# Kernel tuning notes

Measured on AMD Instinct MI355X. Metric: run time of the kernel, lower is better.

The kernel has to match this reference:

```python
import jax, jax.numpy as jnp
import numpy as np

# neighbor-sampled node counts per hop level (outermost -> batch)
SIZES = (1363968, 123904, 11264, 1024)
E = (1239040, 112640, 10240)
D_IN, D_H, D_OUT = 128, 256, 64


def _sage(x_src, x_dst, src, dst, Wl, bl, Wr):
    """PyG SAGEConv(aggr='mean') on bipartite (x_src, x_dst) graph."""
    n_dst = x_dst.shape[0]
    agg = jax.ops.segment_sum(x_src[src], dst, num_segments=n_dst)
    cnt = jax.ops.segment_sum(jnp.ones((src.shape[0],), x_src.dtype), dst, num_segments=n_dst)
    mean = agg / jnp.maximum(cnt, 1.0)[:, None]
    return mean @ Wl + bl + x_dst @ Wr  # lin_l(mean) + lin_r(x_dst), lin_r has no bias


def setup_inputs() -> dict:
    key = jax.random.key(0)
    ks = jax.random.split(key, 16)
    inp = {}
    inp["x"] = jax.random.normal(ks[0], (SIZES[0], D_IN), dtype=jnp.float32)
    dims = [(D_IN, D_H), (D_H, D_H), (D_H, D_OUT)]
    for i, (di, do) in enumerate(dims):
        s = 1.0 / np.sqrt(di)
        inp[f"Wl{i}"] = jax.random.uniform(ks[1 + 3 * i], (di, do), jnp.float32, -s, s)
        inp[f"bl{i}"] = jax.random.uniform(ks[2 + 3 * i], (do,), jnp.float32, -s, s)
        inp[f"Wr{i}"] = jax.random.uniform(ks[3 + 3 * i], (di, do), jnp.float32, -s, s)
    for i in range(3):
        inp[f"edge_src{i}"] = jax.random.randint(ks[10 + i * 2], (E[i],), 0, SIZES[i], dtype=jnp.int32)
        inp[f"edge_dst{i}"] = jax.random.randint(ks[11 + i * 2 - 1], (E[i],), 0, SIZES[i + 1], dtype=jnp.int32)
    return inp


def reference(x, Wl0, bl0, Wr0, Wl1, bl1, Wr1, Wl2, bl2, Wr2,
              edge_src0, edge_dst0, edge_src1, edge_dst1, edge_src2, edge_dst2):
    # layer 0 (i=0 != num_layers-1=1 -> relu; dropout is identity in eval)
    h = _sage(x, x[:SIZES[1]], edge_src0, edge_dst0, Wl0, bl0, Wr0)
    h = jax.nn.relu(h)
    # layer 1 (i=1 == num_layers-1 -> no relu)
    h = _sage(h, h[:SIZES[2]], edge_src1, edge_dst1, Wl1, bl1, Wr1)
    # layer 2 (i=2 != 1 -> relu, faithful to the original quirk)
    h = _sage(h, h[:SIZES[3]], edge_src2, edge_dst2, Wl2, bl2, Wr2)
    h = jax.nn.relu(h)
    return h
```

## Files before the change

### kernel.cpp

```cpp
#include <hip/hip_runtime.h>

#define SZ0 1363968
#define SZ1 123904
#define SZ2 11264
#define SZ3 1024
#define NE0 1239040
#define NE1 112640
#define NE2 10240
#define DIN 128
#define DH  256
#define DOUT 64

__global__ __launch_bounds__(256) void hist_all(
    const int* __restrict__ ed0, const int* __restrict__ ed1,
    const int* __restrict__ ed2, int* __restrict__ bk0,
    int* __restrict__ bk1, int* __restrict__ bk2)
{
    int e = blockIdx.x * 256 + threadIdx.x;
    if (e < NE0) {
        atomicAdd(&bk0[ed0[e]], 1);
    } else if (e < NE0 + NE1) {
        atomicAdd(&bk1[ed1[e - NE0]], 1);
    } else {
        atomicAdd(&bk2[ed2[e - NE0 - NE1]], 1);
    }
}

__global__ __launch_bounds__(1024) void scan_all(
    int* __restrict__ a0, int n0, int* __restrict__ a1, int n1,
    int* __restrict__ a2, int n2)
{
    __shared__ int sums[1024];
    int* a; int n;
    if (blockIdx.x == 0)      { a = a0; n = n0; }
    else if (blockIdx.x == 1) { a = a1; n = n1; }
    else                      { a = a2; n = n2; }

    const int t = threadIdx.x;
    const int C = (n + 1023) >> 10;
    const int lo = t * C;
    const int hi = min(lo + C, n);
    int s = 0;
    for (int i = lo; i < hi; i++) s += a[i];
    sums[t] = s;
    __syncthreads();
    for (int off = 1; off < 1024; off <<= 1) {
        int v = (t >= off) ? sums[t - off] : 0;
        __syncthreads();
        sums[t] += v;
        __syncthreads();
    }
    int pre = (t == 0) ? 0 : sums[t - 1];
    for (int i = lo; i < hi; i++) { int v = a[i]; a[i] = pre; pre += v; }
}

__global__ __launch_bounds__(256) void bucket_all(
    const int* __restrict__ es0, const int* __restrict__ ed0,
    const int* __restrict__ es1, const int* __restrict__ ed1,
    const int* __restrict__ es2, const int* __restrict__ ed2,
    int* __restrict__ bk0, int* __restrict__ bk1, int* __restrict__ bk2,
    int* __restrict__ p0, int* __restrict__ p1, int* __restrict__ p2)
{
    int e = blockIdx.x * 256 + threadIdx.x;
    if (e < NE0) {
        int pos = atomicAdd(&bk0[ed0[e]], 1);
        p0[pos] = es0[e];
    } else if (e < NE0 + NE1) {
        int i = e - NE0;
        int pos = atomicAdd(&bk1[ed1[i]], 1);
        p1[pos] = es1[i];
    } else {
        int i = e - NE0 - NE1;
        int pos = atomicAdd(&bk2[ed2[i]], 1);
        p2[pos] = es2[i];
    }
}

template <int D>
__global__ __launch_bounds__(256) void gather_mean(
    const float* __restrict__ X, const int* __restrict__ perm,
    const int* __restrict__ ends, float* __restrict__ out)
{
    constexpr int VEC = D / 64;
    const int wave = (blockIdx.x * 256 + threadIdx.x) >> 6;
    const int lane = threadIdx.x & 63;
    const int start = (wave == 0) ? 0 : ends[wave - 1];
    const int end = ends[wave];

    float acc[4][VEC];
#pragma unroll
    for (int u = 0; u < 4; u++)
#pragma unroll
        for (int i = 0; i < VEC; i++) acc[u][i] = 0.0f;

    int e = start;
    for (; e + 4 <= end; e += 4) {
        int s0 = perm[e], s1 = perm[e + 1], s2 = perm[e + 2], s3 = perm[e + 3];
        const float* p0 = X + (size_t)s0 * D + lane * VEC;
        const float* p1 = X + (size_t)s1 * D + lane * VEC;
        const float* p2 = X + (size_t)s2 * D + lane * VEC;
        const float* p3 = X + (size_t)s3 * D + lane * VEC;
        if (VEC == 2) {
            float2 v0 = *reinterpret_cast<const float2*>(p0);
            float2 v1 = *reinterpret_cast<const float2*>(p1);
            float2 v2 = *reinterpret_cast<const float2*>(p2);
            float2 v3 = *reinterpret_cast<const float2*>(p3);
            acc[0][0] += v0.x; acc[0][1] += v0.y;
            acc[1][0] += v1.x; acc[1][1] += v1.y;
            acc[2][0] += v2.x; acc[2][1] += v2.y;
            acc[3][0] += v3.x; acc[3][1] += v3.y;
        } else {
            float4 v0 = *reinterpret_cast<const float4*>(p0);
            float4 v1 = *reinterpret_cast<const float4*>(p1);
            float4 v2 = *reinterpret_cast<const float4*>(p2);
            float4 v3 = *reinterpret_cast<const float4*>(p3);
            acc[0][0] += v0.x; acc[0][1] += v0.y; acc[0][2] += v0.z; acc[0][3] += v0.w;
            acc[1][0] += v1.x; acc[1][1] += v1.y; acc[1][2] += v1.z; acc[1][3] += v1.w;
            acc[2][0] += v2.x; acc[2][1] += v2.y; acc[2][2] += v2.z; acc[2][3] += v2.w;
            acc[3][0] += v3.x; acc[3][1] += v3.y; acc[3][2] += v3.z; acc[3][3] += v3.w;
        }
    }
    for (; e < end; e++) {
        int s0 = perm[e];
        const float* p0 = X + (size_t)s0 * D + lane * VEC;
        if (VEC == 2) {
            float2 v0 = *reinterpret_cast<const float2*>(p0);
            acc[0][0] += v0.x; acc[0][1] += v0.y;
        } else {
            float4 v0 = *reinterpret_cast<const float4*>(p0);
            acc[0][0] += v0.x; acc[0][1] += v0.y; acc[0][2] += v0.z; acc[0][3] += v0.w;
        }
    }

    const float inv = 1.0f / (float)max(end - start, 1);
    float* o = out + (size_t)wave * D + lane * VEC;
    if (VEC == 2) {
        float2 v;
        v.x = (acc[0][0] + acc[1][0] + acc[2][0] + acc[3][0]) * inv;
        v.y = (acc[0][1] + acc[1][1] + acc[2][1] + acc[3][1]) * inv;
        *reinterpret_cast<float2*>(o) = v;
    } else {
        float4 v;
        v.x = (acc[0][0] + acc[1][0] + acc[2][0] + acc[3][0]) * inv;
        v.y = (acc[0][1] + acc[1][1] + acc[2][1] + acc[3][1]) * inv;
        v.z = (acc[0][2] + acc[1][2] + acc[2][2] + acc[3][2]) * inv;
        v.w = (acc[0][3] + acc[1][3] + acc[2][3] + acc[3][3]) * inv;
        *reinterpret_cast<float4*>(o) = v;
    }
}

template <int BM, int BN>
__global__ __launch_bounds__(256) void gemm_sage(
    const float* __restrict__ A1, const float* __restrict__ A2,
    const float* __restrict__ B1, const float* __restrict__ B2,
    const float* __restrict__ bias, float* __restrict__ C,
    int K1, int K2, int do_relu)
{
    constexpr int BK = 32;
    constexpr int ROWS = BM / 16;
    constexpr int G = BN / 64;
    constexpr int AF4 = (BM * 8) / 256;
    constexpr int BF4 = (BN * 8) / 256;

    __shared__ float As[BK][BM + 4];
    __shared__ float Bs[BK][BN + 4];

    const int tid = threadIdx.x;
    const int m0 = blockIdx.x * BM;
    const int ty = tid >> 4;
    const int tx = tid & 15;

    float acc[ROWS][G * 4];
#pragma unroll
    for (int i = 0; i < ROWS; i++)
#pragma unroll
        for (int j = 0; j < G * 4; j++) acc[i][j] = 0.0f;

    const int K = K1 + K2;
    for (int kt = 0; kt < K; kt += BK) {
        const float* Ap; const float* Bp; int lK, kof;
        if (kt < K1) { Ap = A1; Bp = B1; lK = K1; kof = kt; }
        else         { Ap = A2; Bp = B2; lK = K2; kof = kt - K1; }

#pragma unroll
        for (int j = 0; j < AF4; j++) {
            int id = tid * AF4 + j;
            int m = id >> 3;
            int q = id & 7;
            float4 v = *reinterpret_cast<const float4*>(
                Ap + (size_t)(m0 + m) * lK + kof + q * 4);
            As[q * 4 + 0][m] = v.x;
            As[q * 4 + 1][m] = v.y;
            As[q * 4 + 2][m] = v.z;
            As[q * 4 + 3][m] = v.w;
        }
#pragma unroll
        for (int j = 0; j < BF4; j++) {
            int id = tid * BF4 + j;
            int k = id / (BN / 4);
            int c = id % (BN / 4);
            float4 v = *reinterpret_cast<const float4*>(
                Bp + (size_t)(kof + k) * BN + c * 4);
            *reinterpret_cast<float4*>(&Bs[k][c * 4]) = v;
        }
        __syncthreads();

#pragma unroll
        for (int kk = 0; kk < BK; kk++) {
            float a[ROWS];
            if constexpr (ROWS == 4) {
                float4 av = *reinterpret_cast<const float4*>(&As[kk][ty * 4]);
                a[0] = av.x; a[1] = av.y; a[2] = av.z; a[3] = av.w;
            } else {
                float2 av = *reinterpret_cast<const float2*>(&As[kk][ty * 2]);
                a[0] = av.x; a[1] = av.y;
            }
#pragma unroll
            for (int g = 0; g < G; g++) {
                float4 bv = *reinterpret_cast<const float4*>(&Bs[kk][g * 64 + tx * 4]);
                const float b[4] = {bv.x, bv.y, bv.z, bv.w};
#pragma unroll
                for (int i = 0; i < ROWS; i++)
#pragma unroll
                    for (int jj = 0; jj < 4; jj++)
                        acc[i][g * 4 + jj] += a[i] * b[jj];
            }
        }
        __syncthreads();
    }

#pragma unroll
    for (int i = 0; i < ROWS; i++) {
        const int row = m0 + ty * ROWS + i;
#pragma unroll
        for (int g = 0; g < G; g++) {
            const float4 bb = *reinterpret_cast<const float4*>(bias + g * 64 + tx * 4);
            float v0 = acc[i][g * 4 + 0] + bb.x;
            float v1 = acc[i][g * 4 + 1] + bb.y;
            float v2 = acc[i][g * 4 + 2] + bb.z;
            float v3 = acc[i][g * 4 + 3] + bb.w;
            if (do_relu) {
                v0 = fmaxf(v0, 0.0f); v1 = fmaxf(v1, 0.0f);
                v2 = fmaxf(v2, 0.0f); v3 = fmaxf(v3, 0.0f);
            }
            float4 o; o.x = v0; o.y = v1; o.z = v2; o.w = v3;
            *reinterpret_cast<float4*>(C + (size_t)row * BN + g * 64 + tx * 4) = o;
        }
    }
}

extern "C" void kernel_launch(void* const* d_in, const int* in_sizes, int n_in,
                              void* d_out, int out_size, void* d_ws, size_t ws_size,
                              hipStream_t stream)
{
    const float* x   = (const float*)d_in[0];
    const float* Wl0 = (const float*)d_in[1];
    const float* bl0 = (const float*)d_in[2];
    const float* Wr0 = (const float*)d_in[3];
    const float* Wl1 = (const float*)d_in[4];
    const float* bl1 = (const float*)d_in[5];
    const float* Wr1 = (const float*)d_in[6];
    const float* Wl2 = (const float*)d_in[7];
    const float* bl2 = (const float*)d_in[8];
    const float* Wr2 = (const float*)d_in[9];
    const int* es0 = (const int*)d_in[10];
    const int* ed0 = (const int*)d_in[11];
    const int* es1 = (const int*)d_in[12];
    const int* ed1 = (const int*)d_in[13];
    const int* es2 = (const int*)d_in[14];
    const int* ed2 = (const int*)d_in[15];

    int* bk0   = (int*)d_ws;
    int* bk1   = bk0 + SZ1;
    int* bk2   = bk1 + SZ2;
    int* perm0 = bk2 + SZ3;
    int* perm1 = perm0 + NE0;
    int* perm2 = perm1 + NE1;
    float* agg0 = (float*)(perm2 + NE2);
    float* agg1 = agg0 + (size_t)SZ1 * DIN;
    float* agg2 = agg1 + (size_t)SZ2 * DH;
    float* h1   = agg2 + (size_t)SZ3 * DH;
    float* h2   = agg0;

    hipMemsetAsync(bk0, 0, (size_t)(SZ1 + SZ2 + SZ3) * sizeof(int), stream);

    constexpr int NET = NE0 + NE1 + NE2;
    hist_all<<<NET / 256, 256, 0, stream>>>(ed0, ed1, ed2, bk0, bk1, bk2);
    scan_all<<<3, 1024, 0, stream>>>(bk0, SZ1, bk1, SZ2, bk2, SZ3);
    bucket_all<<<NET / 256, 256, 0, stream>>>(es0, ed0, es1, ed1, es2, ed2,
                                              bk0, bk1, bk2, perm0, perm1, perm2);

    gather_mean<DIN><<<SZ1 / 4, 256, 0, stream>>>(x, perm0, bk0, agg0);
    gemm_sage<64, DH><<<SZ1 / 64, 256, 0, stream>>>(
        agg0, x, Wl0, Wr0, bl0, h1, DIN, DIN, 1);

    gather_mean<DH><<<SZ2 / 4, 256, 0, stream>>>(h1, perm1, bk1, agg1);
    gemm_sage<32, DH><<<SZ2 / 32, 256, 0, stream>>>(
        agg1, h1, Wl1, Wr1, bl1, h2, DH, DH, 0);

    gather_mean<DH><<<SZ3 / 4, 256, 0, stream>>>(h2, perm2, bk2, agg2);
    gemm_sage<32, DOUT><<<SZ3 / 32, 256, 0, stream>>>(
        agg2, h2, Wl2, Wr2, bl2, (float*)d_out, DH, DH, 1);
}
```

Baseline: 1.608 ms.

## Use split-bf16 MFMA for layer-0 SAGE GEMM

Replaces the FP32 SIMT GEMM for layer 0 with a matrix-core kernel that splits each fp32 operand into high and low bf16 parts and accumulates three bf16 MFMA products to approximate fp32 accuracy. The weights are pre-converted into a packed hi/lo layout by a small new kernel. The activations are converted in-kernel into XOR-swizzled shared memory. The aim is to cut the compute cost of the largest GEMM, at the price of extra conversion work and slightly lower precision than true fp32.

After: 1.533 ms. 4.6% less time.

```diff
diff --git a/kernel.cpp b/kernel.cpp
--- a/kernel.cpp
+++ b/kernel.cpp
@@ -10,6 +10,35 @@
 #define DIN 128
 #define DH  256
 #define DOUT 64
+
+typedef __attribute__((ext_vector_type(8))) short bf16x8;
+typedef __attribute__((ext_vector_type(4))) float f32x4;
+
+__device__ __forceinline__ unsigned short f2bf(float f) {
+    unsigned u = __float_as_uint(f);
+    u += 0x7FFF + ((u >> 16) & 1);
+    return (unsigned short)(u >> 16);
+}
+__device__ __forceinline__ float bf2f(unsigned short h) {
+    return __uint_as_float(((unsigned)h) << 16);
+}
+
+__global__ __launch_bounds__(256) void bconv0(
+    const float* __restrict__ Wl, const float* __restrict__ Wr,
+    unsigned short* __restrict__ Bh, unsigned short* __restrict__ Bl)
+{
+    int id = blockIdx.x * 256 + threadIdx.x;
+    int h = id >> 15;
+    int k = (id >> 8) & 127;
+    int n = id & 255;
+    float w = (h ? Wr : Wl)[k * 256 + n];
+    unsigned short hv = f2bf(w);
+    unsigned short lv = f2bf(w - bf2f(hv));
+    int c = k >> 5, kbl = (k >> 3) & 3, j = k & 7;
+    int addr = (((h * 4 + c) * 4 + kbl) * 256 + n) * 8 + j;
+    Bh[addr] = hv;
+    Bl[addr] = lv;
+}
 
 __global__ __launch_bounds__(256) void hist_all(
     const int* __restrict__ ed0, const int* __restrict__ ed1,
@@ -149,6 +178,112 @@
     }
 }
 
+__global__ __launch_bounds__(256) void gemm_sage0_mfma(
+    const float* __restrict__ A1, const float* __restrict__ A2,
+    const unsigned short* __restrict__ Bh_ws,
+    const unsigned short* __restrict__ Bl_ws,
+    const float* __restrict__ bias, float* __restrict__ C)
+{
+    __shared__ unsigned short Ah[64 * 128];
+    __shared__ unsigned short Al[64 * 128];
+    __shared__ unsigned short Bh[4 * 256 * 8];
+    __shared__ unsigned short Bl[4 * 256 * 8];
+
+    const int tid = threadIdx.x;
+    const int m0 = blockIdx.x * 64;
+    const int w = tid >> 6;
+    const int lane = tid & 63;
+    const int lg = lane >> 4;
+    const int lr = lane & 15;
+
+    f32x4 acc[4][4];
+#pragma unroll
+    for (int i = 0; i < 4; i++)
+#pragma unroll
+        for (int j = 0; j < 4; j++) acc[i][j] = (f32x4){0.f, 0.f, 0.f, 0.f};
+
+    for (int h = 0; h < 2; h++) {
+        const float* Asrc = h ? A2 : A1;
+        for (int c = 0; c < 4; c++) {
+            __syncthreads();
+            if (c == 0) {
+#pragma unroll
+                for (int j = 0; j < 8; j++) {
+                    int id = j * 256 + tid;
+                    int m = id >> 5;
+                    int q = id & 31;
+                    float4 v = *reinterpret_cast<const float4*>(
+                        Asrc + (size_t)(m0 + m) * 128 + q * 4);
+                    unsigned short h0 = f2bf(v.x), h1 = f2bf(v.y);
+                    unsigned short h2 = f2bf(v.z), h3 = f2bf(v.w);
+                    int off = (m * 256 + q * 8) ^ ((m & 7) << 4);
+                    *reinterpret_cast<short4*>((char*)Ah + off) =
+                        make_short4((short)h0, (short)h1, (short)h2, (short)h3);
+                    short4 ls;
+                    ls.x = (short)f2bf(v.x - bf2f(h0));
+                    ls.y = (short)f2bf(v.y - bf2f(h1));
+                    ls.z = (short)f2bf(v.z - bf2f(h2));
+                    ls.w = (short)f2bf(v.w - bf2f(h3));
+                    *reinterpret_cast<short4*>((char*)Al + off) = ls;
+                }
+            }
+            {
+                const float4* sh = reinterpret_cast<const float4*>(
+                    Bh_ws + (size_t)(h * 4 + c) * 8192);
+                const float4* sl = reinterpret_cast<const float4*>(
+                    Bl_ws + (size_t)(h * 4 + c) * 8192);
+#pragma unroll
+                for (int j = 0; j < 4; j++) {
+                    int id = j * 256 + tid;
+                    *reinterpret_cast<float4*>(&Bh[id * 8]) = sh[id];
+                    *reinterpret_cast<float4*>(&Bl[id * 8]) = sl[id];
+                }
+            }
+            __syncthreads();
+
+            bf16x8 ah[4], al[4];
+#pragma unroll
+            for (int mt = 0; mt < 4; mt++) {
+                int row = mt * 16 + lr;
+                int off = (row * 256 + (c * 4 + lg) * 16) ^ ((row & 7) << 4);
+                ah[mt] = *reinterpret_cast<const bf16x8*>((const char*)Ah + off);
+                al[mt] = *reinterpret_cast<const bf16x8*>((const char*)Al + off);
+            }
+#pragma unroll
+            for (int nt = 0; nt < 4; nt++) {
+                int bo = (lg * 256 + w * 64 + nt * 16 + lr) * 8;
+                bf16x8 bh = *reinterpret_cast<const bf16x8*>(&Bh[bo]);
+                bf16x8 bl = *reinterpret_cast<const bf16x8*>(&Bl[bo]);
+#pragma unroll
+                for (int mt = 0; mt < 4; mt++) {
+                    acc[mt][nt] = __builtin_amdgcn_mfma_f32_16x16x32_bf16(
+                        ah[mt], bh, acc[mt][nt], 0, 0, 0);
+                    acc[mt][nt] = __builtin_amdgcn_mfma_f32_16x16x32_bf16(
+                        ah[mt], bl, acc[mt][nt], 0, 0, 0);
+                    acc[mt][nt] = __builtin_amdgcn_mfma_f32_16x16x32_bf16(
+                        al[mt], bh, acc[mt][nt], 0, 0, 0);
+                }
+            }
+        }
+    }
+
+#pragma unroll
+    for (int nt = 0; nt < 4; nt++) {
+        const int n = w * 64 + nt * 16 + lr;
+        const float bv = bias[n];
+#pragma unroll
+        for (int mt = 0; mt < 4; mt++) {
+#pragma unroll
+            for (int r = 0; r < 4; r++) {
+                const int row = m0 + mt * 16 + lg * 4 + r;
+                float v = acc[mt][nt][r] + bv;
+                v = fmaxf(v, 0.0f);
+                C[(size_t)row * 256 + n] = v;
+            }
+        }
+    }
+}
+
 template <int BM, int BN>
 __global__ __launch_bounds__(256) void gemm_sage(
     const float* __restrict__ A1, const float* __restrict__ A2,
@@ -281,8 +416,12 @@
     float* agg2 = agg1 + (size_t)SZ2 * DH;
     float* h1   = agg2 + (size_t)SZ3 * DH;
     float* h2   = agg0;
+    unsigned short* bwsh = (unsigned short*)(h1 + (size_t)SZ1 * DH);
+    unsigned short* bwsl = bwsh + 65536;
 
     hipMemsetAsync(bk0, 0, (size_t)(SZ1 + SZ2 + SZ3) * sizeof(int), stream);
+
+    bconv0<<<256, 256, 0, stream>>>(Wl0, Wr0, bwsh, bwsl);
 
     constexpr int NET = NE0 + NE1 + NE2;
     hist_all<<<NET / 256, 256, 0, stream>>>(ed0, ed1, ed2, bk0, bk1, bk2);
@@ -291,8 +430,7 @@
                                               bk0, bk1, bk2, perm0, perm1, perm2);
 
     gather_mean<DIN><<<SZ1 / 4, 256, 0, stream>>>(x, perm0, bk0, agg0);
-    gemm_sage<64, DH><<<SZ1 / 64, 256, 0, stream>>>(
-        agg0, x, Wl0, Wr0, bl0, h1, DIN, DIN, 1);
+    gemm_sage0_mfma<<<SZ1 / 64, 256, 0, stream>>>(agg0, x, bwsh, bwsl, bl0, h1);
 
     gather_mean<DH><<<SZ2 / 4, 256, 0, stream>>>(h1, perm1, bk1, agg1);
     gemm_sage<32, DH><<<SZ2 / 32, 256, 0, stream>>>(
```
